# Kernel optimization log

Measured on AMD Instinct MI355X. Metric: run time of the kernel, lower is better.

Reference implementation:

```python
import jax, jax.numpy as jnp
import numpy as np

THETA = 0.5
LEAF_SIZE = 32
N_ATOMS = 8192
N_GRAPHS = 2


def _build_tree(pos_np, indices):
    # Mirrors OpenBoundaryTreeLongRangeKernel._build_tree (octree split at bbox center).
    local = pos_np[indices]
    cmin = local.min(axis=0)
    cmax = local.max(axis=0)
    center = 0.5 * (cmin + cmax)
    half = float((cmax - cmin).max() * 0.5)
    node = {"indices": indices, "iset": set(indices), "center": center,
            "half": half, "children": [], "cid": -1}
    if len(indices) <= LEAF_SIZE:
        return node
    bins = {}
    for i in indices:
        p = pos_np[i]
        key = (int(p[0] >= center[0]), int(p[1] >= center[1]), int(p[2] >= center[2]))
        bins.setdefault(key, []).append(i)
    if len(bins) <= 1:
        return node  # degenerate split -> treated as leaf (is_leaf == no children)
    node["children"] = [_build_tree(pos_np, ci) for ci in bins.values()]
    return node


def _plan(pos_np, batch_np, n_graphs, soft):
    # Host-side Barnes-Hut traversal (the torch original does this with .item() syncs).
    # Emits flat (target, source) direct pairs and (target, cluster) monopole pairs.
    direct_t, direct_s, clus_t, clus_c = [], [], [], []
    clusters = []
    for g in range(n_graphs):
        idx = np.nonzero(batch_np == g)[0]
        if idx.size == 0:
            continue
        root = _build_tree(pos_np, [int(i) for i in idx])
        for t in idx:
            t = int(t)
            tpos = pos_np[t]
            stack = [root]
            while stack:
                node = stack.pop()
                if not node["children"]:  # leaf: direct near-field sum
                    for s in node["indices"]:
                        if s != t:
                            direct_t.append(t)
                            direct_s.append(s)
                    continue
                d = tpos - node["center"]
                dist = float(np.sqrt((d * d).sum() + soft * soft))
                diam = max(2.0 * node["half"], 1e-9)
                if (t not in node["iset"]) and (diam / dist < THETA):
                    if node["cid"] < 0:
                        node["cid"] = len(clusters)
                        clusters.append(node["indices"])
                    clus_t.append(t)
                    clus_c.append(node["cid"])
                else:
                    stack.extend(node["children"])
    if clusters:
        midx = np.concatenate([np.asarray(c, dtype=np.int32) for c in clusters])
        mseg = np.concatenate([np.full(len(c), i, np.int32) for i, c in enumerate(clusters)])
        mcnt = np.asarray([len(c) for c in clusters], dtype=np.float32)
    else:
        midx = np.zeros((0,), np.int32)
        mseg = np.zeros((0,), np.int32)
        mcnt = np.ones((1,), np.float32)
    return (np.asarray(direct_t, np.int32), np.asarray(direct_s, np.int32),
            np.asarray(clus_t, np.int32), np.asarray(clus_c, np.int32),
            midx, mseg, mcnt, max(len(clusters), 1))


def _energy(pos, source, screening, softening, plan, n_atoms):
    # Vectorized, differentiable evaluation of the planned interactions.
    dt, ds, ct, cc, midx, mseg, mcnt, n_clusters = plan
    soft2 = softening * softening
    phi = jnp.zeros((n_atoms,), dtype=pos.dtype)
    if dt.size:
        delta = pos[dt] - pos[ds]                       # [P,3]
        r = jnp.sqrt(jnp.sum(delta * delta, axis=-1) + soft2)
        phi = phi + jax.ops.segment_sum(source[ds] * jnp.exp(-screening * r) / r,
                                        dt, num_segments=n_atoms)
    if ct.size:
        q = jax.ops.segment_sum(source[midx], mseg, num_segments=n_clusters)
        center = (jax.ops.segment_sum(pos[midx], mseg, num_segments=n_clusters)
                  / jnp.asarray(mcnt)[:, None])          # differentiable cluster mean
        delta = pos[ct] - center[cc]                    # [C,3]
        r = jnp.sqrt(jnp.sum(delta * delta, axis=-1) + soft2)
        phi = phi + jax.ops.segment_sum(q[cc] * jnp.exp(-screening * r) / r,
                                        ct, num_segments=n_atoms)
    return 0.5 * (source * phi)[:, None]                # [N,1], energy_partition='potential'


def setup_inputs() -> dict:
    key = jax.random.key(0)
    k1, k2, k3 = jax.random.split(key, 3)
    pos = jax.random.normal(k1, (N_ATOMS, 3), dtype=jnp.float32) * 6.0
    batch = jnp.sort(jax.random.randint(k2, (N_ATOMS,), 0, N_GRAPHS)).astype(jnp.int32)
    cell = jnp.zeros((N_GRAPHS, 3, 3), dtype=jnp.float32)
    source = jax.random.normal(k3, (N_ATOMS,), dtype=jnp.float32)
    screening = jnp.float32(0.5)
    softening = jnp.float32(0.1)
    return {"pos": pos, "batch": batch, "cell": cell, "source": source,
            "screening": screening, "softening": softening}


def reference(pos, batch, cell, source, screening, softening):
    pos_np = np.asarray(pos, dtype=np.float32)
    batch_np = np.asarray(batch)
    plan = _plan(pos_np, batch_np, int(cell.shape[0]), float(np.asarray(softening)))
    return _energy(pos, source, screening, softening, plan, pos.shape[0])
```

## Files before the change

kernel.cpp:

```cpp
#include <hip/hip_runtime.h>

#define LEAF_SZ 32
#define MAXN 16384
#define MAXNODES 65536
#define ARENA_BASE 32768
#define MAXG 64
#define NQ 1024
#define PCAP 224
#define BGRID 128
#define LCAP 256
#define LSTK 192
#define BSTK 32
#define WQCAP 64

struct __align__(64) TNode { int4 meta; float4 c4; float4 m4; float4 pad; };

__device__ int    g_perm[MAXN];
__device__ int    g_ptmp[MAXN];
__device__ float4 g_p4[MAXN];
__device__ float4 g_t4[MAXN];
__device__ int    g_nstart[MAXNODES];
__device__ int    g_nend[MAXNODES];
__device__ TNode  g_nodes[MAXNODES];
__device__ int    g_root[MAXG];
__device__ int    g_ncount;
__device__ int    g_lrange[8];
__device__ int    g_done[4];

struct NodeSh {
    float  mn[4][3], mx[4][3];
    double sx[4], sy[4], sz[4], sq[4];
    int    c8[4][8];
    int    cur[8];
    float  cc[3];
    int    info;
    int    base, num;
    int    tot[8], offk[8];
};

__device__ __forceinline__ void process_node2(NodeSh& sh, int n, int st, int en)
{
    const int tid  = threadIdx.x;
    const int wid  = tid >> 6;
    const int lane = tid & 63;
    const int cnt = en - st;

    float mnx = 3.402823466e38f, mny = mnx, mnz = mnx;
    float mxx = -mnx, mxy = -mnx, mxz = -mnx;
    double sx = 0.0, sy = 0.0, sz = 0.0, sq = 0.0;
    for (int j = st + tid; j < en; j += 256) {
        float4 p = g_p4[j];
        mnx = fminf(mnx, p.x); mny = fminf(mny, p.y); mnz = fminf(mnz, p.z);
        mxx = fmaxf(mxx, p.x); mxy = fmaxf(mxy, p.y); mxz = fmaxf(mxz, p.z);
        sx += (double)p.x; sy += (double)p.y; sz += (double)p.z; sq += (double)p.w;
    }
    for (int o = 1; o < 64; o <<= 1) {
        mnx = fminf(mnx, __shfl_xor(mnx, o));
        mny = fminf(mny, __shfl_xor(mny, o));
        mnz = fminf(mnz, __shfl_xor(mnz, o));
        mxx = fmaxf(mxx, __shfl_xor(mxx, o));
        mxy = fmaxf(mxy, __shfl_xor(mxy, o));
        mxz = fmaxf(mxz, __shfl_xor(mxz, o));
        sx += __shfl_xor(sx, o);
        sy += __shfl_xor(sy, o);
        sz += __shfl_xor(sz, o);
        sq += __shfl_xor(sq, o);
    }
    if (lane == 0) {
        sh.mn[wid][0] = mnx; sh.mn[wid][1] = mny; sh.mn[wid][2] = mnz;
        sh.mx[wid][0] = mxx; sh.mx[wid][1] = mxy; sh.mx[wid][2] = mxz;
        sh.sx[wid] = sx; sh.sy[wid] = sy; sh.sz[wid] = sz; sh.sq[wid] = sq;
    }
    __syncthreads();
    if (tid == 0) {
        float a0 = sh.mn[0][0], a1 = sh.mn[0][1], a2 = sh.mn[0][2];
        float b0 = sh.mx[0][0], b1 = sh.mx[0][1], b2 = sh.mx[0][2];
        double tx = sh.sx[0], ty = sh.sy[0], tz = sh.sz[0], tq = sh.sq[0];
        for (int w = 1; w < 4; ++w) {
            a0 = fminf(a0, sh.mn[w][0]); a1 = fminf(a1, sh.mn[w][1]); a2 = fminf(a2, sh.mn[w][2]);
            b0 = fmaxf(b0, sh.mx[w][0]); b1 = fmaxf(b1, sh.mx[w][1]); b2 = fmaxf(b2, sh.mx[w][2]);
            tx += sh.sx[w]; ty += sh.sy[w]; tz += sh.sz[w]; tq += sh.sq[w];
        }
        float cx = 0.5f * (a0 + b0), cy = 0.5f * (a1 + b1), cz = 0.5f * (a2 + b2);
        g_nodes[n].c4 = make_float4(cx, cy, cz, 0.5f * fmaxf(fmaxf(b0 - a0, b1 - a1), b2 - a2));
        const float fc = (float)cnt;
        g_nodes[n].m4 = make_float4((float)tx / fc, (float)ty / fc, (float)tz / fc, (float)tq);
        sh.cc[0] = cx; sh.cc[1] = cy; sh.cc[2] = cz;
        if (cnt <= LEAF_SZ) { g_nodes[n].meta = make_int4(st, en, 0, 0); sh.info = -1; }
        else sh.info = 0;
    }
    __syncthreads();
    if (sh.info < 0) return;
    const float cx = sh.cc[0], cy = sh.cc[1], cz = sh.cc[2];

    int c8[8] = {0,0,0,0,0,0,0,0};
    for (int j = st + tid; j < en; j += 256) {
        float4 p = g_p4[j];
        int oct = (p.x >= cx ? 1 : 0) | (p.y >= cy ? 2 : 0) | (p.z >= cz ? 4 : 0);
        c8[oct]++;
    }
    #pragma unroll
    for (int k = 0; k < 8; ++k)
        for (int o = 1; o < 64; o <<= 1)
            c8[k] += __shfl_xor(c8[k], o);
    if (lane == 0)
        #pragma unroll
        for (int k = 0; k < 8; ++k) sh.c8[wid][k] = c8[k];
    __syncthreads();
    if (tid == 0) {
        int tot[8], nonempty = 0;
        #pragma unroll
        for (int k = 0; k < 8; ++k) {
            tot[k] = sh.c8[0][k] + sh.c8[1][k] + sh.c8[2][k] + sh.c8[3][k];
            nonempty += (tot[k] > 0) ? 1 : 0;
        }
        if (nonempty <= 1) { g_nodes[n].meta = make_int4(st, en, 0, 0); sh.info = -1; }
        else {
            int base = atomicAdd(&g_ncount, nonempty);
            int acc = st, ci = base;
            #pragma unroll
            for (int k = 0; k < 8; ++k) {
                sh.cur[k] = acc;
                sh.offk[k] = acc - st;
                sh.tot[k] = tot[k];
                if (tot[k] > 0) { g_nstart[ci] = acc; g_nend[ci] = acc + tot[k]; ++ci; }
                acc += tot[k];
            }
            g_nodes[n].meta = make_int4(st, en, base, nonempty);
            sh.base = base; sh.num = nonempty; sh.info = 1;
        }
    }
    __syncthreads();
    if (sh.info < 0) return;

    for (int j = st + tid; j < en; j += 256) {
        float4 p = g_p4[j];
        int id = g_perm[j];
        int oct = (p.x >= cx ? 1 : 0) | (p.y >= cy ? 2 : 0) | (p.z >= cz ? 4 : 0);
        int pdst = atomicAdd(&sh.cur[oct], 1);
        g_ptmp[pdst] = id; g_t4[pdst] = p;
    }
    __syncthreads();
    for (int j = st + tid; j < en; j += 256) {
        g_perm[j] = g_ptmp[j];
        g_p4[j]   = g_t4[j];
    }
    __syncthreads();
}

__global__ __launch_bounds__(256)
void initroots_kernel(const float* __restrict__ pos, const float* __restrict__ src,
                      const int* __restrict__ batch, int N, int n_graphs)
{
    __shared__ int s_first[MAXG], s_end[MAXG];
    const int tid = threadIdx.x;
    int i = blockIdx.x * 256 + tid;
    if (i < N) {
        g_perm[i] = i;
        g_p4[i] = make_float4(pos[3*i], pos[3*i+1], pos[3*i+2], src[i]);
    }
    if (blockIdx.x != 0) return;

    for (int g = tid; g < MAXG; g += 256) { s_first[g] = -1; s_end[g] = 0; }
    __syncthreads();
    for (int j = tid; j < N; j += 256) {
        int b = batch[j];
        if (j == 0     || batch[j-1] != b) s_first[b] = j;
        if (j == N - 1 || batch[j+1] != b) s_end[b]   = j + 1;
    }
    __syncthreads();
    if (tid == 0) {
        int nc = 0;
        for (int g = 0; g < n_graphs && g < MAXG; ++g) {
            if (s_first[g] >= 0) {
                g_root[g] = nc;
                g_nstart[nc] = s_first[g];
                g_nend[nc]   = s_end[g];
                ++nc;
            } else g_root[g] = -1;
        }
        g_ncount = nc;
        g_lrange[0] = 0; g_lrange[1] = nc;
        g_done[0] = g_done[1] = g_done[2] = g_done[3] = 0;
    }
}

__global__ __launch_bounds__(256) void level_kernel(int lev)
{
    __shared__ NodeSh sh;
    const int lb = g_lrange[lev], le = g_lrange[lev + 1];
    for (int n = lb + blockIdx.x; n < le; n += BGRID) {
        __syncthreads();
        process_node2(sh, n, g_nstart[n], g_nend[n]);
    }
    __syncthreads();
    if (threadIdx.x == 0) {
        __threadfence();
        int d = atomicAdd(&g_done[lev], 1);
        if (d == BGRID - 1)
            g_lrange[lev + 2] = atomicAdd(&g_ncount, 0);
    }
}

__device__ __forceinline__ void lds_subtree(int rootn, int st, int en, int abase,
                                            float4* a4, int* aid,
                                            int* lid, int* la, int* lbb)
{
    const int lane = threadIdx.x & 63;
    const int cnt = en - st;
    const unsigned long long mlt = (1ull << lane) - 1ull;

    for (int j = lane; j < cnt; j += 64) {
        a4[j]  = g_p4[st + j];
        aid[j] = g_perm[st + j];
    }
    asm volatile("s_waitcnt vmcnt(0) lgkmcnt(0)" ::: "memory");
    __builtin_amdgcn_wave_barrier();

    int sp = 0;
    int cn = rootn, ca = 0, cb = cnt;
    while (true) {
        const int c = cb - ca;
        float4 pv[4]; int idv[4]; int oc[4];
        float mnx = 3.402823466e38f, mny = mnx, mnz = mnx;
        float mxx = -mnx, mxy = -mnx, mxz = -mnx;
        float sx = 0.f, sy = 0.f, sz = 0.f, sq = 0.f;
        #pragma unroll
        for (int i = 0; i < 4; ++i) {
            bool act = (i*64 + lane) < c;
            int j = act ? (ca + i*64 + lane) : ca;
            float4 p = a4[j];
            pv[i] = p; idv[i] = aid[j];
            if (act) {
                mnx = fminf(mnx, p.x); mny = fminf(mny, p.y); mnz = fminf(mnz, p.z);
                mxx = fmaxf(mxx, p.x); mxy = fmaxf(mxy, p.y); mxz = fmaxf(mxz, p.z);
                sx += p.x; sy += p.y; sz += p.z; sq += p.w;
            }
        }
        for (int o = 1; o < 64; o <<= 1) {
            mnx = fminf(mnx, __shfl_xor(mnx, o));
            mny = fminf(mny, __shfl_xor(mny, o));
            mnz = fminf(mnz, __shfl_xor(mnz, o));
            mxx = fmaxf(mxx, __shfl_xor(mxx, o));
            mxy = fmaxf(mxy, __shfl_xor(mxy, o));
            mxz = fmaxf(mxz, __shfl_xor(mxz, o));
            sx += __shfl_xor(sx, o);
            sy += __shfl_xor(sy, o);
            sz += __shfl_xor(sz, o);
            sq += __shfl_xor(sq, o);
        }
        const float cx = 0.5f * (mnx + mxx);
        const float cy = 0.5f * (mny + mxy);
        const float cz = 0.5f * (mnz + mxz);
        if (lane == 0) {
            g_nodes[cn].c4 = make_float4(cx, cy, cz, 0.5f * fmaxf(fmaxf(mxx - mnx, mxy - mny), mxz - mnz));
            const float fc = (float)c;
            g_nodes[cn].m4 = make_float4(sx / fc, sy / fc, sz / fc, sq);
        }

        int nonempty = 0;
        int c8[8] = {0,0,0,0,0,0,0,0};
        if (c > LEAF_SZ) {
            #pragma unroll
            for (int i = 0; i < 4; ++i) {
                bool act = (i*64 + lane) < c;
                int o = act ? ((pv[i].x >= cx ? 1 : 0) | (pv[i].y >= cy ? 2 : 0) | (pv[i].z >= cz ? 4 : 0)) : 8;
                oc[i] = o;
                #pragma unroll
                for (int k = 0; k < 8; ++k)
                    c8[k] += (int)__popcll(__ballot(o == k));
            }
            #pragma unroll
            for (int k = 0; k < 8; ++k) nonempty += (c8[k] > 0) ? 1 : 0;
        }

        if (c <= LEAF_SZ || nonempty <= 1) {
            if (lane == 0) g_nodes[cn].meta = make_int4(st + ca, st + cb, 0, 0);
        } else {
            int off[8], acc = 0;
            #pragma unroll
            for (int k = 0; k < 8; ++k) { off[k] = acc; acc += c8[k]; }
            if (lane == 0) g_nodes[cn].meta = make_int4(st + ca, st + cb, abase, nonempty);
            int cum[8] = {0,0,0,0,0,0,0,0};
            #pragma unroll
            for (int i = 0; i < 4; ++i) {
                int o = oc[i];
                int pdst = 0;
                #pragma unroll
                for (int k = 0; k < 8; ++k) {
                    unsigned long long b = __ballot(o == k);
                    if (o == k) pdst = ca + off[k] + cum[k] + (int)__popcll(b & mlt);
                    cum[k] += (int)__popcll(b);
                }
                if (o < 8) { a4[pdst] = pv[i]; aid[pdst] = idv[i]; }
            }
            asm volatile("s_waitcnt lgkmcnt(0)" ::: "memory");
            __builtin_amdgcn_wave_barrier();
            if (lane == 0) {
                int ci = 0;
                #pragma unroll
                for (int k = 0; k < 8; ++k) {
                    if (c8[k] > 0) {
                        lid[sp + ci] = abase + ci;
                        la [sp + ci] = ca + off[k];
                        lbb[sp + ci] = ca + off[k] + c8[k];
                        ++ci;
                    }
                }
            }
            abase += nonempty; sp += nonempty;
            if (sp > LSTK) sp = LSTK;
        }
        if (sp <= 0) break;
        --sp;
        __builtin_amdgcn_wave_barrier();
        asm volatile("s_waitcnt lgkmcnt(0)" ::: "memory");
        cn = lid[sp]; ca = la[sp]; cb = lbb[sp];
        __builtin_amdgcn_wave_barrier();
    }

    for (int j = lane; j < cnt; j += 64) {
        g_p4[st + j]  = a4[j];
        g_perm[st + j] = aid[j];
    }
    asm volatile("s_waitcnt vmcnt(0)" ::: "memory");
}

__global__ __launch_bounds__(256) void block_subtree_kernel()
{
    __shared__ NodeSh sh;
    __shared__ int bs_id[BSTK], bs_st[BSTK], bs_en[BSTK];
    __shared__ int wq_id[WQCAP], wq_st[WQCAP], wq_en[WQCAP];
    __shared__ int s_bsp, s_wq;
    __shared__ float4 s_a4[4][LCAP];
    __shared__ int    s_aid[4][LCAP];
    __shared__ int    s_lid[4][LSTK], s_la[4][LSTK], s_lb[4][LSTK];

    const int tid = threadIdx.x;
    const int wid = tid >> 6;
    const int lb = g_lrange[2], le = g_lrange[3];

    for (int task = lb + blockIdx.x; task < le; task += BGRID) {
        __syncthreads();
        if (tid == 0) {
            int st = g_nstart[task], en = g_nend[task];
            if (en - st <= LCAP) { wq_id[0] = task; wq_st[0] = st; wq_en[0] = en; s_wq = 1; s_bsp = 0; }
            else                 { bs_id[0] = task; bs_st[0] = st; bs_en[0] = en; s_bsp = 1; s_wq = 0; }
        }
        __syncthreads();

        while (true) {
            __syncthreads();
            const int bsp = s_bsp;
            if (bsp == 0) break;
            const int n  = bs_id[bsp-1];
            const int st = bs_st[bsp-1];
            const int en = bs_en[bsp-1];
            __syncthreads();
            if (tid == 0) s_bsp = bsp - 1;
            process_node2(sh, n, st, en);
            if (tid == 0 && sh.info == 1) {
                int ci = 0;
                #pragma unroll
                for (int k = 0; k < 8; ++k) {
                    if (sh.tot[k] > 0) {
                        int cst = st + sh.offk[k], cen = cst + sh.tot[k];
                        int cid = sh.base + ci; ++ci;
                        if (cen - cst <= LCAP) {
                            if (s_wq < WQCAP) { wq_id[s_wq] = cid; wq_st[s_wq] = cst; wq_en[s_wq] = cen; ++s_wq; }
                        } else {
                            if (s_bsp < BSTK) { bs_id[s_bsp] = cid; bs_st[s_bsp] = cst; bs_en[s_bsp] = cen; ++s_bsp; }
                        }
                    }
                }
            }
        }
        __syncthreads();

        const int nwq = s_wq;
        float4* a4 = s_a4[wid];  int* aid = s_aid[wid];
        int* lid = s_lid[wid];   int* la = s_la[wid];  int* lbb = s_lb[wid];
        for (int i = wid; i < nwq; i += 4) {
            int cid = wq_id[i], cst = wq_st[i], cen = wq_en[i];
            lds_subtree(cid, cst, cen, ARENA_BASE + 2 * cst, a4, aid, lid, la, lbb);
        }
    }
}

__global__ __launch_bounds__(256)
void traverse_kernel(const int* __restrict__ batch,
                     const float* __restrict__ p_scr, const float* __restrict__ p_soft,
                     float* __restrict__ out, int N)
{
    __shared__ int s_q[4][NQ];
    __shared__ int s_pj[4][PCAP];
    __shared__ int s_qt[4];
    const int wid  = threadIdx.x >> 6;
    const int lane = threadIdx.x & 63;
    const int slot = blockIdx.x * 4 + wid;
    if (slot >= N) return;
    const int t = g_perm[slot];

    const float scr   = p_scr[0];
    const float soft  = p_soft[0];
    const float soft2 = soft * soft;
    const float cexp  = -scr * 1.4426950408889634f;
    const float4 tp = g_p4[slot];
    const float tx = tp.x, ty = tp.y, tz = tp.z;
    const int inv_t = slot;

    volatile int* q  = s_q[wid];
    volatile int* pj = s_pj[wid];
    if (lane == 0) { q[0] = g_root[batch[t]]; s_qt[wid] = 1; }
    __builtin_amdgcn_wave_barrier();

    float phi = 0.f;
    int qh = 0;
    while (true) {
        __builtin_amdgcn_wave_barrier();
        int qt = ((volatile int*)s_qt)[wid];
        if (qh >= qt) break;
        int take = qt - qh; if (take > 64) take = 64;
        int node = (lane < take) ? q[(qh + lane) & (NQ - 1)] : -1;
        qh += take;

        int leaf_st = 0, leaf_cnt = 0;
        if (node >= 0) {
            const int4 meta = g_nodes[node].meta;
            if (meta.w == 0) {
                leaf_st = meta.x; leaf_cnt = meta.y - meta.x;
            } else {
                float4 c4 = g_nodes[node].c4;
                float dx = tx - c4.x, dy = ty - c4.y, dz = tz - c4.z;
                float dist = sqrtf(dx*dx + dy*dy + dz*dz + soft2);
                float diam = fmaxf(2.0f * c4.w, 1e-9f);
                bool inside = (inv_t >= meta.x) && (inv_t < meta.y);
                if (!inside && diam < 0.5f * dist) {
                    float4 m4 = g_nodes[node].m4;
                    float ax = tx - m4.x, ay = ty - m4.y, az = tz - m4.z;
                    float s = ax*ax + ay*ay + az*az + soft2;
                    float rinv = rsqrtf(s);
                    phi += m4.w * exp2f(cexp * (s * rinv)) * rinv;
                } else {
                    int p = atomicAdd(&s_qt[wid], meta.w);
                    for (int c = 0; c < meta.w; ++c) q[(p + c) & (NQ - 1)] = meta.z + c;
                }
            }
        }

        bool hasself = (inv_t >= leaf_st) && (inv_t < leaf_st + leaf_cnt);
        int cnt_adj = leaf_cnt - (hasself ? 1 : 0);
        int x = cnt_adj;
        #pragma unroll
        for (int o = 1; o < 64; o <<= 1) { int y = __shfl_up(x, o); if (lane >= o) x += y; }
        int total = __shfl(x, 63);
        int off = x - cnt_adj;
        int selfpos = hasself ? (inv_t - leaf_st) : 0x7fffffff;

        for (int cb = 0; cb < total; cb += PCAP) {
            int ce = cb + PCAP; if (ce > total) ce = total;
            int ws = off > cb ? off : cb;
            int we = (off + cnt_adj) < ce ? (off + cnt_adj) : ce;
            for (int w = ws; w < we; ++w) {
                int i = w - off;
                pj[w - cb] = leaf_st + i + (i >= selfpos ? 1 : 0);
            }
            __builtin_amdgcn_wave_barrier();
            int cnum = ce - cb;
            for (int p = lane; p < cnum; p += 64) {
                int j = pj[p];
                float4 pp = g_p4[j];
                float dx = tx - pp.x, dy = ty - pp.y, dz = tz - pp.z;
                float s = dx*dx + dy*dy + dz*dz + soft2;
                float rinv = rsqrtf(s);
                phi += pp.w * exp2f(cexp * (s * rinv)) * rinv;
            }
            __builtin_amdgcn_wave_barrier();
        }
    }

    #pragma unroll
    for (int o = 1; o < 64; o <<= 1) phi += __shfl_xor(phi, o);
    if (lane == 0) out[t] = 0.5f * (tp.w * phi);
}

extern "C" void kernel_launch(void* const* d_in, const int* in_sizes, int n_in,
                              void* d_out, int out_size, void* d_ws, size_t ws_size,
                              hipStream_t stream) {
    const float* pos    = (const float*)d_in[0];
    const int*   batch  = (const int*)  d_in[1];
    const float* source = (const float*)d_in[3];
    const float* p_scr  = (const float*)d_in[4];
    const float* p_soft = (const float*)d_in[5];

    const int N        = in_sizes[0] / 3;
    const int n_graphs = in_sizes[2] / 9;

    initroots_kernel<<<(N + 255) / 256, 256, 0, stream>>>(pos, source, batch, N, n_graphs);
    level_kernel<<<BGRID, 256, 0, stream>>>(0);
    level_kernel<<<BGRID, 256, 0, stream>>>(1);
    block_subtree_kernel<<<BGRID, 256, 0, stream>>>();

    const int blocks = (N + 3) / 4;
    traverse_kernel<<<blocks, 256, 0, stream>>>(batch, p_scr, p_soft, (float*)d_out, N);
}
```

Measured before the change: 177.8 us.

## Fuse root init with level-0 split and replace serial leaf pair expansion

Result: faster. 151.9 us (-14.6%).

```diff
diff --git a/kernel.cpp b/kernel.cpp
--- a/kernel.cpp
+++ b/kernel.cpp
@@ -6,12 +6,12 @@
 #define ARENA_BASE 32768
 #define MAXG 64
 #define NQ 1024
-#define PCAP 224
 #define BGRID 128
 #define LCAP 256
 #define LSTK 192
 #define BSTK 32
 #define WQCAP 64
+#define NW0 16
 
 struct __align__(64) TNode { int4 meta; float4 c4; float4 m4; float4 pad; };
 
@@ -24,8 +24,8 @@
 __device__ TNode  g_nodes[MAXNODES];
 __device__ int    g_root[MAXG];
 __device__ int    g_ncount;
-__device__ int    g_lrange[8];
-__device__ int    g_done[4];
+__device__ int    g_lrange[4];
+__device__ int    g_done[2];
 
 struct NodeSh {
     float  mn[4][3], mx[4][3];
@@ -148,57 +148,181 @@
     __syncthreads();
 }
 
-__global__ __launch_bounds__(256)
-void initroots_kernel(const float* __restrict__ pos, const float* __restrict__ src,
-                      const int* __restrict__ batch, int N, int n_graphs)
+__global__ __launch_bounds__(1024)
+void level0_kernel(const float* __restrict__ pos, const float* __restrict__ src,
+                   const int* __restrict__ batch, int N, int n_graphs)
 {
-    __shared__ int s_first[MAXG], s_end[MAXG];
-    const int tid = threadIdx.x;
-    int i = blockIdx.x * 256 + tid;
-    if (i < N) {
-        g_perm[i] = i;
-        g_p4[i] = make_float4(pos[3*i], pos[3*i+1], pos[3*i+2], src[i]);
-    }
-    if (blockIdx.x != 0) return;
-
-    for (int g = tid; g < MAXG; g += 256) { s_first[g] = -1; s_end[g] = 0; }
-    __syncthreads();
-    for (int j = tid; j < N; j += 256) {
-        int b = batch[j];
-        if (j == 0     || batch[j-1] != b) s_first[b] = j;
-        if (j == N - 1 || batch[j+1] != b) s_end[b]   = j + 1;
+    __shared__ int    s_first[MAXG], s_end[MAXG];
+    __shared__ float  s_mn[NW0][3], s_mx[NW0][3];
+    __shared__ double s_sx[NW0], s_sy[NW0], s_sz[NW0], s_sq[NW0];
+    __shared__ int    s_c8[NW0][8];
+    __shared__ int    s_cur[8];
+    __shared__ float  s_cc[3];
+    __shared__ int    s_info;
+    const int tid = threadIdx.x, wid = tid >> 6, lane = tid & 63;
+    const int ng = (n_graphs < MAXG) ? n_graphs : MAXG;
+
+    for (int g = tid; g < MAXG; g += 1024) { s_first[g] = -1; s_end[g] = 0; }
+    __syncthreads();
+    for (int i = tid; i < N; i += 1024) {
+        int b = batch[i];
+        if (i == 0     || batch[i-1] != b) s_first[b] = i;
+        if (i == N - 1 || batch[i+1] != b) s_end[b]   = i + 1;
+    }
+    __syncthreads();
+
+    const int g = blockIdx.x;
+    int nc = 0, myroot = -1;
+    for (int q = 0; q < ng; ++q)
+        if (s_first[q] >= 0) { if (q == g) myroot = nc; ++nc; }
+    const int nb = nc + 8 * ng;
+
+    if (g == 0 && tid == 0) {
+        int r = 0;
+        for (int q = 0; q < ng; ++q) {
+            if (s_first[q] >= 0) g_root[q] = r++;
+            else {
+                g_root[q] = -1;
+                for (int c = 0; c < 8; ++c) g_nstart[nc + q*8 + c] = -1;
+            }
+        }
+        g_ncount = nb;
+        g_lrange[0] = nc;
+        g_lrange[1] = nb;
+        g_done[1] = 0;
+    }
+    if (g >= ng || myroot < 0) return;
+
+    const int st = s_first[g], en = s_end[g];
+    const int cnt = en - st;
+    const int n = myroot;
+    const int cbase = nc + g * 8;
+
+    float mnx = 3.402823466e38f, mny = mnx, mnz = mnx;
+    float mxx = -mnx, mxy = -mnx, mxz = -mnx;
+    double sx = 0.0, sy = 0.0, sz = 0.0, sq = 0.0;
+    for (int j = st + tid; j < en; j += 1024) {
+        float x = pos[3*j], y = pos[3*j+1], z = pos[3*j+2], s = src[j];
+        mnx = fminf(mnx, x); mny = fminf(mny, y); mnz = fminf(mnz, z);
+        mxx = fmaxf(mxx, x); mxy = fmaxf(mxy, y); mxz = fmaxf(mxz, z);
+        sx += (double)x; sy += (double)y; sz += (double)z; sq += (double)s;
+    }
+    for (int o = 1; o < 64; o <<= 1) {
+        mnx = fminf(mnx, __shfl_xor(mnx, o));
+        mny = fminf(mny, __shfl_xor(mny, o));
+        mnz = fminf(mnz, __shfl_xor(mnz, o));
+        mxx = fmaxf(mxx, __shfl_xor(mxx, o));
+        mxy = fmaxf(mxy, __shfl_xor(mxy, o));
+        mxz = fmaxf(mxz, __shfl_xor(mxz, o));
+        sx += __shfl_xor(sx, o);
+        sy += __shfl_xor(sy, o);
+        sz += __shfl_xor(sz, o);
+        sq += __shfl_xor(sq, o);
+    }
+    if (lane == 0) {
+        s_mn[wid][0] = mnx; s_mn[wid][1] = mny; s_mn[wid][2] = mnz;
+        s_mx[wid][0] = mxx; s_mx[wid][1] = mxy; s_mx[wid][2] = mxz;
+        s_sx[wid] = sx; s_sy[wid] = sy; s_sz[wid] = sz; s_sq[wid] = sq;
     }
     __syncthreads();
     if (tid == 0) {
-        int nc = 0;
-        for (int g = 0; g < n_graphs && g < MAXG; ++g) {
-            if (s_first[g] >= 0) {
-                g_root[g] = nc;
-                g_nstart[nc] = s_first[g];
-                g_nend[nc]   = s_end[g];
-                ++nc;
-            } else g_root[g] = -1;
-        }
-        g_ncount = nc;
-        g_lrange[0] = 0; g_lrange[1] = nc;
-        g_done[0] = g_done[1] = g_done[2] = g_done[3] = 0;
+        float a0 = s_mn[0][0], a1 = s_mn[0][1], a2 = s_mn[0][2];
+        float b0 = s_mx[0][0], b1 = s_mx[0][1], b2 = s_mx[0][2];
+        double tx = s_sx[0], ty = s_sy[0], tz = s_sz[0], tq = s_sq[0];
+        for (int w = 1; w < NW0; ++w) {
+            a0 = fminf(a0, s_mn[w][0]); a1 = fminf(a1, s_mn[w][1]); a2 = fminf(a2, s_mn[w][2]);
+            b0 = fmaxf(b0, s_mx[w][0]); b1 = fmaxf(b1, s_mx[w][1]); b2 = fmaxf(b2, s_mx[w][2]);
+            tx += s_sx[w]; ty += s_sy[w]; tz += s_sz[w]; tq += s_sq[w];
+        }
+        float cx = 0.5f * (a0 + b0), cy = 0.5f * (a1 + b1), cz = 0.5f * (a2 + b2);
+        g_nodes[n].c4 = make_float4(cx, cy, cz, 0.5f * fmaxf(fmaxf(b0 - a0, b1 - a1), b2 - a2));
+        const float fc = (float)cnt;
+        g_nodes[n].m4 = make_float4((float)tx / fc, (float)ty / fc, (float)tz / fc, (float)tq);
+        s_cc[0] = cx; s_cc[1] = cy; s_cc[2] = cz;
+        s_info = (cnt <= LEAF_SZ) ? -1 : 0;
+        if (s_info < 0) g_nodes[n].meta = make_int4(st, en, 0, 0);
+    }
+    __syncthreads();
+
+    if (s_info == 0) {
+        const float cx = s_cc[0], cy = s_cc[1], cz = s_cc[2];
+        int c8[8] = {0,0,0,0,0,0,0,0};
+        for (int j = st + tid; j < en; j += 1024) {
+            int oct = (pos[3*j] >= cx ? 1 : 0) | (pos[3*j+1] >= cy ? 2 : 0) | (pos[3*j+2] >= cz ? 4 : 0);
+            c8[oct]++;
+        }
+        #pragma unroll
+        for (int k = 0; k < 8; ++k)
+            for (int o = 1; o < 64; o <<= 1)
+                c8[k] += __shfl_xor(c8[k], o);
+        if (lane == 0)
+            #pragma unroll
+            for (int k = 0; k < 8; ++k) s_c8[wid][k] = c8[k];
+        __syncthreads();
+        if (tid == 0) {
+            int tot[8], nonempty = 0;
+            #pragma unroll
+            for (int k = 0; k < 8; ++k) {
+                int tk = 0;
+                for (int w = 0; w < NW0; ++w) tk += s_c8[w][k];
+                tot[k] = tk;
+                nonempty += (tk > 0) ? 1 : 0;
+            }
+            if (nonempty <= 1) {
+                g_nodes[n].meta = make_int4(st, en, 0, 0);
+                for (int c = 0; c < 8; ++c) g_nstart[cbase + c] = -1;
+                s_info = -1;
+            } else {
+                int acc = st, ci = cbase;
+                #pragma unroll
+                for (int k = 0; k < 8; ++k) {
+                    s_cur[k] = acc;
+                    if (tot[k] > 0) { g_nstart[ci] = acc; g_nend[ci] = acc + tot[k]; ++ci; }
+                    acc += tot[k];
+                }
+                for (int c = ci; c < cbase + 8; ++c) g_nstart[c] = -1;
+                g_nodes[n].meta = make_int4(st, en, cbase, nonempty);
+                s_info = 1;
+            }
+        }
+        __syncthreads();
+    } else if (tid == 0) {
+        for (int c = 0; c < 8; ++c) g_nstart[cbase + c] = -1;
+    }
+
+    if (s_info == 1) {
+        const float cx = s_cc[0], cy = s_cc[1], cz = s_cc[2];
+        for (int j = st + tid; j < en; j += 1024) {
+            float x = pos[3*j], y = pos[3*j+1], z = pos[3*j+2], s = src[j];
+            int oct = (x >= cx ? 1 : 0) | (y >= cy ? 2 : 0) | (z >= cz ? 4 : 0);
+            int pdst = atomicAdd(&s_cur[oct], 1);
+            g_p4[pdst] = make_float4(x, y, z, s);
+            g_perm[pdst] = j;
+        }
+    } else {
+        for (int j = st + tid; j < en; j += 1024) {
+            g_p4[j] = make_float4(pos[3*j], pos[3*j+1], pos[3*j+2], src[j]);
+            g_perm[j] = j;
+        }
     }
 }
 
-__global__ __launch_bounds__(256) void level_kernel(int lev)
+__global__ __launch_bounds__(256) void level1_kernel()
 {
     __shared__ NodeSh sh;
-    const int lb = g_lrange[lev], le = g_lrange[lev + 1];
+    const int lb = g_lrange[0], le = g_lrange[1];
     for (int n = lb + blockIdx.x; n < le; n += BGRID) {
         __syncthreads();
-        process_node2(sh, n, g_nstart[n], g_nend[n]);
+        int st = g_nstart[n];
+        if (st < 0) continue;
+        process_node2(sh, n, st, g_nend[n]);
     }
     __syncthreads();
     if (threadIdx.x == 0) {
         __threadfence();
-        int d = atomicAdd(&g_done[lev], 1);
+        int d = atomicAdd(&g_done[1], 1);
         if (d == BGRID - 1)
-            g_lrange[lev + 2] = atomicAdd(&g_ncount, 0);
+            g_lrange[2] = atomicAdd(&g_ncount, 0);
     }
 }
 
@@ -338,7 +462,7 @@
 
     const int tid = threadIdx.x;
     const int wid = tid >> 6;
-    const int lb = g_lrange[2], le = g_lrange[3];
+    const int lb = g_lrange[1], le = g_lrange[2];
 
     for (int task = lb + blockIdx.x; task < le; task += BGRID) {
         __syncthreads();
@@ -393,7 +517,7 @@
                      float* __restrict__ out, int N)
 {
     __shared__ int s_q[4][NQ];
-    __shared__ int s_pj[4][PCAP];
+    __shared__ int s_sb[4][64], s_ss[4][64], s_mk[4][64];
     __shared__ int s_qt[4];
     const int wid  = threadIdx.x >> 6;
     const int lane = threadIdx.x & 63;
@@ -409,8 +533,10 @@
     const float tx = tp.x, ty = tp.y, tz = tp.z;
     const int inv_t = slot;
 
-    volatile int* q  = s_q[wid];
-    volatile int* pj = s_pj[wid];
+    volatile int* q = s_q[wid];
+    int* sb = s_sb[wid];
+    int* ss = s_ss[wid];
+    int* mk = s_mk[wid];
     if (lane == 0) { q[0] = g_root[batch[t]]; s_qt[wid] = 1; }
     __builtin_amdgcn_wave_barrier();
 
@@ -455,27 +581,39 @@
         for (int o = 1; o < 64; o <<= 1) { int y = __shfl_up(x, o); if (lane >= o) x += y; }
         int total = __shfl(x, 63);
         int off = x - cnt_adj;
-        int selfpos = hasself ? (inv_t - leaf_st) : 0x7fffffff;
-
-        for (int cb = 0; cb < total; cb += PCAP) {
-            int ce = cb + PCAP; if (ce > total) ce = total;
-            int ws = off > cb ? off : cb;
-            int we = (off + cnt_adj) < ce ? (off + cnt_adj) : ce;
-            for (int w = ws; w < we; ++w) {
-                int i = w - off;
-                pj[w - cb] = leaf_st + i + (i >= selfpos ? 1 : 0);
-            }
+
+        if (total > 0) {
+            sb[lane] = leaf_st - off;
+            ss[lane] = hasself ? (off + (inv_t - leaf_st)) : 0x7fffffff;
+            asm volatile("s_waitcnt lgkmcnt(0)" ::: "memory");
             __builtin_amdgcn_wave_barrier();
-            int cnum = ce - cb;
-            for (int p = lane; p < cnum; p += 64) {
-                int j = pj[p];
-                float4 pp = g_p4[j];
-                float dx = tx - pp.x, dy = ty - pp.y, dz = tz - pp.z;
-                float s = dx*dx + dy*dy + dz*dz + soft2;
-                float rinv = rsqrtf(s);
-                phi += pp.w * exp2f(cexp * (s * rinv)) * rinv;
-            }
-            __builtin_amdgcn_wave_barrier();
+            int carry = -1;
+            for (int cb = 0; cb < total; cb += 64) {
+                mk[lane] = -1;
+                asm volatile("s_waitcnt lgkmcnt(0)" ::: "memory");
+                __builtin_amdgcn_wave_barrier();
+                if (cnt_adj > 0 && off >= cb && off < cb + 64) mk[off - cb] = lane;
+                asm volatile("s_waitcnt lgkmcnt(0)" ::: "memory");
+                __builtin_amdgcn_wave_barrier();
+                int own = mk[lane];
+                if (lane == 0) own = own > carry ? own : carry;
+                #pragma unroll
+                for (int o = 1; o < 64; o <<= 1) {
+                    int y = __shfl_up(own, o);
+                    if (lane >= o) own = own > y ? own : y;
+                }
+                carry = __shfl(own, 63);
+                int p = cb + lane;
+                if (p < total) {
+                    int j = sb[own] + p + ((p >= ss[own]) ? 1 : 0);
+                    float4 pp = g_p4[j];
+                    float dx = tx - pp.x, dy = ty - pp.y, dz = tz - pp.z;
+                    float s = dx*dx + dy*dy + dz*dz + soft2;
+                    float rinv = rsqrtf(s);
+                    phi += pp.w * exp2f(cexp * (s * rinv)) * rinv;
+                }
+                __builtin_amdgcn_wave_barrier();
+            }
         }
     }
 
@@ -496,9 +634,10 @@
     const int N        = in_sizes[0] / 3;
     const int n_graphs = in_sizes[2] / 9;
 
-    initroots_kernel<<<(N + 255) / 256, 256, 0, stream>>>(pos, source, batch, N, n_graphs);
-    level_kernel<<<BGRID, 256, 0, stream>>>(0);
-    level_kernel<<<BGRID, 256, 0, stream>>>(1);
+    int g0 = n_graphs > 0 ? n_graphs : 1;
+    if (g0 > MAXG) g0 = MAXG;
+    level0_kernel<<<g0, 1024, 0, stream>>>(pos, source, batch, N, n_graphs);
+    level1_kernel<<<BGRID, 256, 0, stream>>>();
     block_subtree_kernel<<<BGRID, 256, 0, stream>>>();
 
     const int blocks = (N + 3) / 4;
```
